# Performance work log

Hardware: AMD Instinct MI355X
Metric: run time of the kernel (lower is better)

The kernel has to match this reference:

```python
import jax, jax.numpy as jnp
from jax import lax
import numpy as np

N_NEURON = 4096
BATCH = 64
N_STEP = 200


def setup_inputs() -> dict:
    key = jax.random.key(0)
    k1, k2, k3 = jax.random.split(key, 3)
    # state_g is a sigmoid output: keep strictly inside (0, 1) for g_inverse's log
    state_g = jax.random.uniform(k1, (BATCH, N_NEURON), dtype=jnp.float32,
                                 minval=0.05, maxval=0.95)
    # Symmetric_Linear init: W ~ N(0, 0.01), symmetrized, zero diagonal
    W = jax.random.normal(k2, (N_NEURON, N_NEURON), dtype=jnp.float32) * 0.01
    W = W + W.T
    W = W - jnp.diag(jnp.diag(W))
    b = jax.random.normal(k3, (N_NEURON,), dtype=jnp.float32) * 0.01
    beta = jnp.ones((N_NEURON,), dtype=jnp.float32) * 10.0
    tau = jnp.ones((N_NEURON,), dtype=jnp.float32)
    dt_train = jnp.float32(0.1)
    return {"state_g": state_g, "W": W, "b": b, "beta": beta, "tau": tau,
            "dt_train": dt_train, "n_step": N_STEP}


def reference(state_g, W, b, beta, tau, dt_train, n_step):
    # max_x = 50 / beta.max()  (original uses .item(); beta is constant so same value)
    max_x = 50.0 / jnp.max(beta)
    # Symmetric_Linear effective weight: (W + W^T)/2 with zero diagonal.
    # Original recomputes this every step; it's step-invariant so hoist it.
    W_sym = (W + W.T) * 0.5 - jnp.diag(jnp.diag(W))
    # g_inverse: x = (1/beta) * log(g / (1 - g))
    state_x = (1.0 / beta) * jnp.log(state_g / (1.0 - state_g))
    alpha = dt_train / tau  # [N]

    def step(carry, _):
        x, g = carry
        pre = g @ W_sym.T + b                       # [B, N] GEMM
        x = alpha * pre + (1.0 - alpha) * x         # leaky update
        x = jnp.clip(x, -max_x, max_x)
        g = jax.nn.sigmoid(beta * x)
        return (x, g), None

    (state_x, state_g), _ = lax.scan(step, (state_x, state_g), None, length=n_step)
    return state_g
```

## Files before the change

### kernel.cpp

```cpp
#include <hip/hip_runtime.h>
#include <hip/hip_bf16.h>

#define MM 64
#define NN 4096
#define KK 4096
#define NSTEP 200

typedef __bf16 bf16x8 __attribute__((ext_vector_type(8)));
typedef float  f32x4  __attribute__((ext_vector_type(4)));

static __device__ __forceinline__ unsigned short f2bf(float f) {
    __hip_bfloat16 h = __float2bfloat16(f);
    return __builtin_bit_cast(unsigned short, h);
}
static __device__ __forceinline__ float bf2f(unsigned short u) {
    __hip_bfloat16 h = __builtin_bit_cast(__hip_bfloat16, u);
    return __bfloat162float(h);
}


__global__ __launch_bounds__(256) void symm_kernel(const float* __restrict__ W,
                                                   unsigned short* __restrict__ Wfh,
                                                   unsigned short* __restrict__ Wfl) {
    __shared__ float T[64][65];
    const int tid = threadIdx.x;
    const int r0 = blockIdx.y * 64, c0 = blockIdx.x * 64;
#pragma unroll
    for (int i = 0; i < 4; ++i) {
        int lin = tid + i * 256;
        int cc  = lin >> 4;
        int r4  = (lin & 15) * 4;
        float4 v = *(const float4*)&W[(size_t)(c0 + cc) * NN + r0 + r4];
        T[cc][r4 + 0] = v.x; T[cc][r4 + 1] = v.y;
        T[cc][r4 + 2] = v.z; T[cc][r4 + 3] = v.w;
    }
    __syncthreads();
#pragma unroll
    for (int i = 0; i < 4; ++i) {
        int lin = tid + i * 256;
        int rr  = lin >> 4;
        int c4  = (lin & 15) * 4;
        float4 v = *(const float4*)&W[(size_t)(r0 + rr) * NN + c0 + c4];
        float d[4] = {v.x, v.y, v.z, v.w};
        ushort4 ohi, olo;
        unsigned short* ph = (unsigned short*)&ohi;
        unsigned short* pl = (unsigned short*)&olo;
#pragma unroll
        for (int j = 0; j < 4; ++j) {
            float sv = 0.5f * (d[j] + T[c4 + j][rr]);
            if (r0 + rr == c0 + c4 + j) sv = 0.0f;
            unsigned short hi = f2bf(sv);
            ph[j] = hi;
            pl[j] = f2bf(sv - bf2f(hi));
        }
        const int n  = r0 + rr;
        const int kg = c0 + c4;
        const int s16 = n >> 4, ln = n & 15;
        const int kc = kg >> 5, q = (kg & 31) >> 3, j0 = kg & 7;
        size_t off = (((size_t)s16 * 128 + kc) * 64 + q * 16 + ln) * 8 + j0;
        *(ushort4*)&Wfh[off] = ohi;
        *(ushort4*)&Wfl[off] = olo;
    }
}

__global__ __launch_bounds__(256) void init_kernel(const float* __restrict__ g_in,
                                                   const float* __restrict__ beta,
                                                   float* __restrict__ x,
                                                   unsigned short* __restrict__ gfh,
                                                   unsigned short* __restrict__ gfl) {
    int idx = blockIdx.x * 256 + threadIdx.x;
    int r = idx >> 12, c = idx & (NN - 1);
    float g = g_in[idx];
    x[idx] = logf(g / (1.0f - g)) / beta[c];
    unsigned short hi = f2bf(g);
    unsigned short lo = f2bf(g - bf2f(hi));
    size_t off = (((size_t)(c >> 5) * 4 + (r >> 4)) * 64 + ((c & 31) >> 3) * 16 + (r & 15)) * 8 + (c & 7);
    gfh[off] = hi;
    gfl[off] = lo;
}

__global__ __launch_bounds__(256) void maxx_kernel(const float* __restrict__ beta,
                                                   float* __restrict__ out) {
    __shared__ float red[256];
    float m = -1e30f;
    for (int i = threadIdx.x; i < NN; i += 256) m = fmaxf(m, beta[i]);
    red[threadIdx.x] = m;
    __syncthreads();
    for (int s = 128; s > 0; s >>= 1) {
        if (threadIdx.x < s) red[threadIdx.x] = fmaxf(red[threadIdx.x], red[threadIdx.x + s]);
        __syncthreads();
    }
    if (threadIdx.x == 0) out[0] = 50.0f / red[0];
}

__global__ __launch_bounds__(1024, 1) void gemm_kernel(
    const unsigned short* __restrict__ gfh,
    const unsigned short* __restrict__ gfl,
    const unsigned short* __restrict__ Wfh,
    const unsigned short* __restrict__ Wfl,
    float* __restrict__ P)
{
    __shared__ float sacc[16][16][65];

    const int tid  = threadIdx.x;
    const int w    = tid >> 6;
    const int lane = tid & 63;
    const int s64  = blockIdx.x >> 2;
    const int kq   = blockIdx.x & 3;
    const int nq   = w & 3;
    const int kq4  = w >> 2;

    f32x4 acc[4] = {};

#pragma unroll
    for (int it = 0; it < 8; ++it) {
        const int kc = kq * 32 + kq4 * 8 + it;
        const size_t aBase = (size_t)kc * 2048 + lane * 8;
        const int n16 = s64 * 4 + nq;
        const size_t bOff = (((size_t)n16 * 128 + kc) * 64 + lane) * 8;
        bf16x8 bh = *(const bf16x8*)&Wfh[bOff];
        bf16x8 bl = *(const bf16x8*)&Wfl[bOff];
        bf16x8 ah[4], al[4];
#pragma unroll
        for (int mq = 0; mq < 4; ++mq) {
            ah[mq] = *(const bf16x8*)&gfh[aBase + (size_t)mq * 512];
            al[mq] = *(const bf16x8*)&gfl[aBase + (size_t)mq * 512];
        }
#pragma unroll
        for (int mq = 0; mq < 4; ++mq) {
            acc[mq] = __builtin_amdgcn_mfma_f32_16x16x32_bf16(ah[mq], bh, acc[mq], 0, 0, 0);
            acc[mq] = __builtin_amdgcn_mfma_f32_16x16x32_bf16(al[mq], bh, acc[mq], 0, 0, 0);
            acc[mq] = __builtin_amdgcn_mfma_f32_16x16x32_bf16(ah[mq], bl, acc[mq], 0, 0, 0);
        }
    }

#pragma unroll
    for (int mq = 0; mq < 4; ++mq)
#pragma unroll
        for (int rg = 0; rg < 4; ++rg)
            sacc[w][mq * 4 + rg][lane] = acc[mq][rg];
    __syncthreads();

    {
        const int m  = tid >> 4;
        const int tt = tid & 15;
        const int mq = m >> 4, qq = (m & 15) >> 2, rg = m & 3;
        const int ridx = mq * 4 + rg;
        const int nq_c = tt >> 2;
        float4 pv;
#pragma unroll
        for (int j = 0; j < 4; ++j) {
            const int cl = qq * 16 + (tt & 3) * 4 + j;
            (&pv.x)[j] = sacc[nq_c][ridx][cl] + sacc[4 + nq_c][ridx][cl]
                       + sacc[8 + nq_c][ridx][cl] + sacc[12 + nq_c][ridx][cl];
        }
        *(float4*)&P[(((size_t)(kq * 64 + s64) * 64 + m) * 64) + tt * 4] = pv;
    }
}

__global__ __launch_bounds__(256) void epi_kernel(
    const float* __restrict__ P,
    float* __restrict__ x,
    unsigned short* __restrict__ gfh_out,
    unsigned short* __restrict__ gfl_out,
    const float* __restrict__ bvec,
    const float* __restrict__ beta,
    const float* __restrict__ tau,
    const float* __restrict__ dt_ptr,
    const float* __restrict__ maxx_ptr,
    float* __restrict__ gout_f32)
{
    const int tid = threadIdx.x;
    const int s64 = blockIdx.x >> 2;
    const int mq4 = blockIdx.x & 3;
    const int m   = mq4 * 16 + (tid >> 4);
    const int tt  = tid & 15;
    const int c0  = tt * 4;
    const int n0  = s64 * 64 + c0;

    const size_t pb = ((size_t)s64 * 64 + m) * 64 + c0;
    float4 p0 = *(const float4*)&P[pb];
    float4 p1 = *(const float4*)&P[(size_t)(1 * 64) * 4096 + pb];
    float4 p2 = *(const float4*)&P[(size_t)(2 * 64) * 4096 + pb];
    float4 p3 = *(const float4*)&P[(size_t)(3 * 64) * 4096 + pb];
    float sum[4] = {p0.x + p1.x + p2.x + p3.x,
                    p0.y + p1.y + p2.y + p3.y,
                    p0.z + p1.z + p2.z + p3.z,
                    p0.w + p1.w + p2.w + p3.w};

    const float dt = *dt_ptr;
    const float mx = *maxx_ptr;
    float4 b0 = *(const float4*)&bvec[n0];
    float4 e0 = *(const float4*)&beta[n0];
    float4 t0 = *(const float4*)&tau[n0];
    float bb[4] = {b0.x, b0.y, b0.z, b0.w};
    float be[4] = {e0.x, e0.y, e0.z, e0.w};
    float tv[4] = {t0.x, t0.y, t0.z, t0.w};

    float* xp = &x[(size_t)m * NN + n0];
    float4 x0 = *(const float4*)xp;
    float xo[4] = {x0.x, x0.y, x0.z, x0.w};

    float gg[4];
    unsigned short vh[4], vl[4];
#pragma unroll
    for (int j = 0; j < 4; ++j) {
        const float al = dt / tv[j];
        float xn = al * (sum[j] + bb[j]) + (1.0f - al) * xo[j];
        xn = fminf(fmaxf(xn, -mx), mx);
        float g = 1.0f / (1.0f + __expf(-be[j] * xn));
        xo[j] = xn;
        gg[j] = g;
        unsigned short hi = f2bf(g);
        vh[j] = hi;
        vl[j] = f2bf(g - bf2f(hi));
    }
    *(float4*)xp = {xo[0], xo[1], xo[2], xo[3]};

    size_t off = (((size_t)(n0 >> 5) * 4 + (m >> 4)) * 64 + ((n0 & 31) >> 3) * 16 + (m & 15)) * 8 + (n0 & 7);
    *(ushort4*)&gfh_out[off] = {vh[0], vh[1], vh[2], vh[3]};
    *(ushort4*)&gfl_out[off] = {vl[0], vl[1], vl[2], vl[3]};

    if (gout_f32)
        *(float4*)&gout_f32[(size_t)m * NN + n0] = {gg[0], gg[1], gg[2], gg[3]};
}

extern "C" void kernel_launch(void* const* d_in, const int* in_sizes, int n_in,
                              void* d_out, int out_size, void* d_ws, size_t ws_size,
                              hipStream_t stream) {
    const float* state_g = (const float*)d_in[0];
    const float* W       = (const float*)d_in[1];
    const float* b       = (const float*)d_in[2];
    const float* beta    = (const float*)d_in[3];
    const float* tau     = (const float*)d_in[4];
    const float* dt      = (const float*)d_in[5];
    float* out = (float*)d_out;

    char* ws = (char*)d_ws;
    const size_t WH = (size_t)KK * NN * 2;
    const size_t XB = (size_t)MM * NN * 4;
    const size_t GB = (size_t)MM * NN * 2;
    const size_t PB = (size_t)4 * 64 * 64 * 64 * 4;
    unsigned short* Wfh = (unsigned short*)ws;
    unsigned short* Wfl = (unsigned short*)(ws + WH);
    float*          x   = (float*)(ws + 2 * WH);
    unsigned short* g0h = (unsigned short*)(ws + 2 * WH + XB);
    unsigned short* g0l = (unsigned short*)(ws + 2 * WH + XB + GB);
    unsigned short* g1h = (unsigned short*)(ws + 2 * WH + XB + 2 * GB);
    unsigned short* g1l = (unsigned short*)(ws + 2 * WH + XB + 3 * GB);
    float*          P   = (float*)(ws + 2 * WH + XB + 4 * GB);
    float*          mxp = (float*)(ws + 2 * WH + XB + 4 * GB + PB);

    symm_kernel<<<dim3(64, 64), 256, 0, stream>>>(W, Wfh, Wfl);
    init_kernel<<<(MM * NN) / 256, 256, 0, stream>>>(state_g, beta, x, g0h, g0l);
    maxx_kernel<<<1, 256, 0, stream>>>(beta, mxp);

    unsigned short *gih = g0h, *gil = g0l, *goh = g1h, *gol = g1l;
    for (int st = 0; st < NSTEP; ++st) {
        float* of = (st == NSTEP - 1) ? out : nullptr;
        gemm_kernel<<<256, 1024, 0, stream>>>(gih, gil, Wfh, Wfl, P);
        epi_kernel<<<256, 256, 0, stream>>>(P, x, goh, gol, b, beta, tau, dt, mxp, of);
        unsigned short* tp;
        tp = gih; gih = goh; goh = tp;
        tp = gil; gil = gol; gol = tp;
    }
}
```

Before: 3.618 ms.

## Give each wave a full 64x64 tile over fewer K chunks with register reuse

Each of the 16 waves now computes the full 64x64 output block (4x4 MFMA tiles) over 2 K-chunks instead of one 16-column strip over 8 chunks. This reuses each A fragment across 4 N tiles and each B fragment across 4 M tiles, which cuts global and L2 loads per MFMA. The reduction across waves is staged through shared memory: waves 8-15 add into the partials written by waves 0-7, then an 8-way sum produces P. The cost is 64 accumulator registers per lane, a larger LDS footprint and an extra barrier.

```diff
diff --git a/kernel.cpp b/kernel.cpp
--- a/kernel.cpp
+++ b/kernel.cpp
@@ -100,59 +100,76 @@
     const unsigned short* __restrict__ Wfl,
     float* __restrict__ P)
 {
-    __shared__ float sacc[16][16][65];
+    __shared__ float sacc[8][16][64][4];
 
     const int tid  = threadIdx.x;
     const int w    = tid >> 6;
     const int lane = tid & 63;
     const int s64  = blockIdx.x >> 2;
     const int kq   = blockIdx.x & 3;
-    const int nq   = w & 3;
-    const int kq4  = w >> 2;
-
-    f32x4 acc[4] = {};
-
-#pragma unroll
-    for (int it = 0; it < 8; ++it) {
-        const int kc = kq * 32 + kq4 * 8 + it;
-        const size_t aBase = (size_t)kc * 2048 + lane * 8;
-        const int n16 = s64 * 4 + nq;
-        const size_t bOff = (((size_t)n16 * 128 + kc) * 64 + lane) * 8;
-        bf16x8 bh = *(const bf16x8*)&Wfh[bOff];
-        bf16x8 bl = *(const bf16x8*)&Wfl[bOff];
-        bf16x8 ah[4], al[4];
+
+    f32x4 acc[4][4] = {};
+
+#pragma unroll
+    for (int it = 0; it < 2; ++it) {
+        const int kc = kq * 32 + w * 2 + it;
+        bf16x8 ah[4], al[4], bh[4], bl[4];
 #pragma unroll
         for (int mq = 0; mq < 4; ++mq) {
-            ah[mq] = *(const bf16x8*)&gfh[aBase + (size_t)mq * 512];
-            al[mq] = *(const bf16x8*)&gfl[aBase + (size_t)mq * 512];
-        }
-#pragma unroll
-        for (int mq = 0; mq < 4; ++mq) {
-            acc[mq] = __builtin_amdgcn_mfma_f32_16x16x32_bf16(ah[mq], bh, acc[mq], 0, 0, 0);
-            acc[mq] = __builtin_amdgcn_mfma_f32_16x16x32_bf16(al[mq], bh, acc[mq], 0, 0, 0);
-            acc[mq] = __builtin_amdgcn_mfma_f32_16x16x32_bf16(ah[mq], bl, acc[mq], 0, 0, 0);
-        }
-    }
-
-#pragma unroll
-    for (int mq = 0; mq < 4; ++mq)
-#pragma unroll
-        for (int rg = 0; rg < 4; ++rg)
-            sacc[w][mq * 4 + rg][lane] = acc[mq][rg];
+            const size_t a = ((size_t)kc * 4 + mq) * 512 + lane * 8;
+            ah[mq] = *(const bf16x8*)&gfh[a];
+            al[mq] = *(const bf16x8*)&gfl[a];
+        }
+#pragma unroll
+        for (int nq = 0; nq < 4; ++nq) {
+            const size_t b = (((size_t)(s64 * 4 + nq) * 128 + kc) * 64 + lane) * 8;
+            bh[nq] = *(const bf16x8*)&Wfh[b];
+            bl[nq] = *(const bf16x8*)&Wfl[b];
+        }
+#pragma unroll
+        for (int mq = 0; mq < 4; ++mq)
+#pragma unroll
+            for (int nq = 0; nq < 4; ++nq) {
+                acc[mq][nq] = __builtin_amdgcn_mfma_f32_16x16x32_bf16(ah[mq], bh[nq], acc[mq][nq], 0, 0, 0);
+                acc[mq][nq] = __builtin_amdgcn_mfma_f32_16x16x32_bf16(al[mq], bh[nq], acc[mq][nq], 0, 0, 0);
+                acc[mq][nq] = __builtin_amdgcn_mfma_f32_16x16x32_bf16(ah[mq], bl[nq], acc[mq][nq], 0, 0, 0);
+            }
+    }
+
+    if (w < 8) {
+#pragma unroll
+        for (int mq = 0; mq < 4; ++mq)
+#pragma unroll
+            for (int nq = 0; nq < 4; ++nq)
+                *(f32x4*)&sacc[w][mq * 4 + nq][lane][0] = acc[mq][nq];
+    }
+    __syncthreads();
+    if (w >= 8) {
+#pragma unroll
+        for (int mq = 0; mq < 4; ++mq)
+#pragma unroll
+            for (int nq = 0; nq < 4; ++nq) {
+                f32x4 old = *(const f32x4*)&sacc[w - 8][mq * 4 + nq][lane][0];
+                *(f32x4*)&sacc[w - 8][mq * 4 + nq][lane][0] = old + acc[mq][nq];
+            }
+    }
     __syncthreads();
 
     {
         const int m  = tid >> 4;
         const int tt = tid & 15;
-        const int mq = m >> 4, qq = (m & 15) >> 2, rg = m & 3;
-        const int ridx = mq * 4 + rg;
-        const int nq_c = tt >> 2;
+        const int mq = m >> 4, q = (m & 15) >> 2, rg = m & 3;
+        const int nq = tt >> 2;
+        const int fi = mq * 4 + nq;
         float4 pv;
 #pragma unroll
         for (int j = 0; j < 4; ++j) {
-            const int cl = qq * 16 + (tt & 3) * 4 + j;
-            (&pv.x)[j] = sacc[nq_c][ridx][cl] + sacc[4 + nq_c][ridx][cl]
-                       + sacc[8 + nq_c][ridx][cl] + sacc[12 + nq_c][ridx][cl];
+            const int cl = q * 16 + (tt & 3) * 4 + j;
+            float v = 0.0f;
+#pragma unroll
+            for (int kh = 0; kh < 8; ++kh)
+                v += sacc[kh][fi][cl][rg];
+            (&pv.x)[j] = v;
         }
         *(float4*)&P[(((size_t)(kq * 64 + s64) * 64 + m) * 64) + tt * 4] = pv;
     }
```

After: 4.172 ms. 1.15x slower.
